# Optimization experiments

Hardware: AMD Instinct MI355X
Metric: run time of the kernel (lower is better)

## Reference

```python
import jax, jax.numpy as jnp
import numpy as np

N, H, W = 4096, 96, 96
C0 = 0.28209479177387814
C1 = 0.4886025119029199
C2 = [1.0925484305920792, -1.0925484305920792, 0.31539156525252005, -1.0925484305920792, 0.5462742152960396]
C3 = [-0.5900435899266435, 2.890611442640554, -0.4570457994644658, 0.3731763325901154, -0.4570457994644658, 1.445305721320277, -0.5900435899266435]


def setup_inputs() -> dict:
    key = jax.random.key(0)
    ks = jax.random.split(key, 6)
    return {
        'pws': jax.random.normal(ks[0], (N, 3), jnp.float32),
        'low_shs': 0.5 * jax.random.normal(ks[1], (N, 3), jnp.float32),
        'high_shs': 0.1 * jax.random.normal(ks[2], (N, 45), jnp.float32),
        'alphas_raw': jax.random.normal(ks[3], (N, 1), jnp.float32),
        'scales_raw': 0.5 * jax.random.normal(ks[4], (N, 3), jnp.float32) - 3.0,
        'rots_raw': jax.random.normal(ks[5], (N, 4), jnp.float32),
        'us': jnp.zeros((N, 2), jnp.float32),
        'Rcw': jnp.eye(3, dtype=jnp.float32),
        'tcw': jnp.array([0.0, 0.0, 4.0], jnp.float32),
        'cam_intr': jnp.array([120.0, 120.0, 48.0, 48.0], jnp.float32),  # fx fy cx cy
    }


def quat_to_rot(q):
    w, x, y, z = q[:, 0], q[:, 1], q[:, 2], q[:, 3]
    return jnp.stack([
        jnp.stack([1 - 2 * (y * y + z * z), 2 * (x * y - w * z), 2 * (x * z + w * y)], -1),
        jnp.stack([2 * (x * y + w * z), 1 - 2 * (x * x + z * z), 2 * (y * z - w * x)], -1),
        jnp.stack([2 * (x * z - w * y), 2 * (y * z + w * x), 1 - 2 * (x * x + y * y)], -1),
    ], -2)  # [N,3,3]


def sh2color(shs, dirs):
    # shs [N,16,3], dirs [N,3] normalized view directions
    x, y, z = dirs[:, 0:1], dirs[:, 1:2], dirs[:, 2:3]
    xx, yy, zz = x * x, y * y, z * z
    xy, yz, xz = x * y, y * z, x * z
    c = C0 * shs[:, 0]
    c = c - C1 * y * shs[:, 1] + C1 * z * shs[:, 2] - C1 * x * shs[:, 3]
    c = (c + C2[0] * xy * shs[:, 4] + C2[1] * yz * shs[:, 5]
         + C2[2] * (2 * zz - xx - yy) * shs[:, 6]
         + C2[3] * xz * shs[:, 7] + C2[4] * (xx - yy) * shs[:, 8])
    c = (c + C3[0] * y * (3 * xx - yy) * shs[:, 9] + C3[1] * xy * z * shs[:, 10]
         + C3[2] * y * (4 * zz - xx - yy) * shs[:, 11]
         + C3[3] * z * (2 * zz - 3 * xx - 3 * yy) * shs[:, 12]
         + C3[4] * x * (4 * zz - xx - yy) * shs[:, 13]
         + C3[5] * z * (xx - yy) * shs[:, 14]
         + C3[6] * x * (xx - 3 * yy) * shs[:, 15])
    return jnp.maximum(c + 0.5, 0.0)  # [N,3]


def _forward(pws, low_shs, high_shs, alphas_raw, scales_raw, rots_raw, Rcw, tcw, cam_intr):
    fx, fy, cx, cy = cam_intr[0], cam_intr[1], cam_intr[2], cam_intr[3]
    alphas = jax.nn.sigmoid(alphas_raw)[:, 0]                 # get_alphas
    scales = jnp.exp(scales_raw)                              # get_scales
    rots = rots_raw / jnp.linalg.norm(rots_raw, axis=1, keepdims=True)  # get_rots
    shs = jnp.concatenate([low_shs, high_shs], axis=1).reshape(-1, 16, 3)

    # --- project ---
    pcs = pws @ Rcw.T + tcw                                   # [N,3] camera coords
    depths = pcs[:, 2]
    zs = jnp.where(depths > 1e-6, depths, 1e-6)
    u = jnp.stack([fx * pcs[:, 0] / zs + cx, fy * pcs[:, 1] / zs + cy], axis=1)

    # --- cov3d = (R S)(R S)^T ---
    M = quat_to_rot(rots) * scales[:, None, :]
    cov3d = M @ jnp.swapaxes(M, 1, 2)                          # [N,3,3]

    # --- cov2d = J W cov3d W^T J^T + 0.3 I ---
    limx, limy = 1.3 * (W / (2.0 * fx)), 1.3 * (H / (2.0 * fy))
    tx = jnp.clip(pcs[:, 0] / zs, -limx, limx) * zs
    ty = jnp.clip(pcs[:, 1] / zs, -limy, limy) * zs
    zero = jnp.zeros_like(zs)
    J = jnp.stack([
        jnp.stack([fx / zs, zero, -fx * tx / (zs * zs)], -1),
        jnp.stack([zero, fy / zs, -fy * ty / (zs * zs)], -1),
    ], -2)                                                     # [N,2,3]
    T = J @ Rcw
    cov2d = T @ cov3d @ jnp.swapaxes(T, 1, 2)
    a = cov2d[:, 0, 0] + 0.3
    b = cov2d[:, 0, 1]
    c2 = cov2d[:, 1, 1] + 0.3

    # --- inverseCov2D + areas (radius of 3-sigma ellipse) ---
    det = a * c2 - b * b
    cinv = jnp.stack([c2, -b, a], axis=1) / det[:, None]       # [N,3]
    mid = 0.5 * (a + c2)
    lam = mid + jnp.sqrt(jnp.maximum(mid * mid - det, 0.1))
    radius = jnp.ceil(3.0 * jnp.sqrt(lam))
    areas = jnp.stack([radius, radius], axis=1)                # [N,2]

    # --- sh2Color ---
    twc = -(Rcw.T @ tcw)
    dirs = pws - twc
    dirs = dirs / jnp.linalg.norm(dirs, axis=1, keepdims=True)
    colors = sh2color(shs, dirs)                               # [N,3]

    # --- splat: depth-sorted alpha compositing ---
    valid = depths > 0.2
    order = jnp.argsort(depths)
    u_s, cinv_s = u[order], cinv[order]
    alpha_s, color_s, valid_s = alphas[order], colors[order], valid[order]

    px = (jnp.arange(W, dtype=jnp.float32))[None, :].repeat(H, 0).reshape(-1)
    py = (jnp.arange(H, dtype=jnp.float32))[:, None].repeat(W, 1).reshape(-1)
    dx = u_s[:, 0:1] - px[None, :]                             # [N,P]
    dy = u_s[:, 1:2] - py[None, :]
    power = -0.5 * (cinv_s[:, 0:1] * dx * dx + cinv_s[:, 2:3] * dy * dy) - cinv_s[:, 1:2] * dx * dy
    ap = jnp.minimum(alpha_s[:, None] * jnp.exp(jnp.minimum(power, 0.0)), 0.99)
    ap = jnp.where((ap >= 1.0 / 255.0) & valid_s[:, None], ap, 0.0)
    logt = jnp.cumsum(jnp.log1p(-ap), axis=0)
    tau = jnp.exp(jnp.concatenate([jnp.zeros((1, ap.shape[1])), logt[:-1]], axis=0))
    wgt = jnp.where(tau > 1e-4, ap * tau, 0.0)                 # [N,P]
    image = jnp.einsum('nc,np->cp', color_s, wgt).reshape(3, H, W)
    return image, areas


def reference(pws, low_shs, high_shs, alphas_raw, scales_raw, rots_raw, us, Rcw, tcw, cam_intr):
    return _forward(pws, low_shs, high_shs, alphas_raw, scales_raw, rots_raw, Rcw, tcw, cam_intr)
```

## Files before the change

kernel.cpp:

```cpp
#include <hip/hip_runtime.h>
#include <hip/hip_bf16.h>
#include <math.h>

#define GS_N 4096
#define IMG_H 96
#define IMG_W 96
#define NPIX (IMG_H * IMG_W)
#define TILE_PX 12
#define TILES_X 8
#define NTILES (TILES_X * TILES_X)
#define WAVES_PER_TILE 36

#define SH_C0 0.28209479177387814f
#define SH_C1 0.4886025119029199f
__device__ __constant__ float kC2[5] = {1.0925484305920792f, -1.0925484305920792f, 0.31539156525252005f, -1.0925484305920792f, 0.5462742152960396f};
__device__ __constant__ float kC3[7] = {-0.5900435899266435f, 2.890611442640554f, -0.4570457994644658f, 0.3731763325901154f, -0.4570457994644658f, 1.445305721320277f, -0.5900435899266435f};

__global__ __launch_bounds__(256) void gs_prep(
    const float* __restrict__ pws, const float* __restrict__ low_shs,
    const float* __restrict__ high_shs, const float* __restrict__ alphas_raw,
    const float* __restrict__ scales_raw, const float* __restrict__ rots_raw,
    const float* __restrict__ Rcw, const float* __restrict__ tcw,
    const float* __restrict__ cam,
    float* __restrict__ areas_out,
    float* __restrict__ depth_ws,
    int*   __restrict__ rank_ws,
    float4* __restrict__ A_uns,
    float4* __restrict__ B_uns,
    float* __restrict__ C_uns,
    float4* __restrict__ D_uns)
{
    int i = blockIdx.x * 256 + threadIdx.x;
    if (i >= GS_N) return;

    rank_ws[i] = 0;

    float fx = cam[0], fy = cam[1], cxi = cam[2], cyi = cam[3];
    float R0 = Rcw[0], R1 = Rcw[1], R2 = Rcw[2];
    float R3 = Rcw[3], R4 = Rcw[4], R5 = Rcw[5];
    float R6 = Rcw[6], R7 = Rcw[7], R8 = Rcw[8];
    float t0 = tcw[0], t1 = tcw[1], t2 = tcw[2];

    float pwx = pws[3*i+0], pwy = pws[3*i+1], pwz = pws[3*i+2];

    float pcx = R0*pwx + R1*pwy + R2*pwz + t0;
    float pcy = R3*pwx + R4*pwy + R5*pwz + t1;
    float pcz = R6*pwx + R7*pwy + R8*pwz + t2;

    float depth = pcz;
    float zs = (depth > 1e-6f) ? depth : 1e-6f;

    float ux = fx * pcx / zs + cxi;
    float uy = fy * pcy / zs + cyi;

    float alpha = 1.0f / (1.0f + expf(-alphas_raw[i]));

    float s0 = expf(scales_raw[3*i+0]);
    float s1 = expf(scales_raw[3*i+1]);
    float s2 = expf(scales_raw[3*i+2]);

    float qw = rots_raw[4*i+0], qx = rots_raw[4*i+1], qy = rots_raw[4*i+2], qz = rots_raw[4*i+3];
    float qn = sqrtf(qw*qw + qx*qx + qy*qy + qz*qz);
    qw /= qn; qx /= qn; qy /= qn; qz /= qn;

    float r00 = 1.0f - 2.0f*(qy*qy + qz*qz);
    float r01 = 2.0f*(qx*qy - qw*qz);
    float r02 = 2.0f*(qx*qz + qw*qy);
    float r10 = 2.0f*(qx*qy + qw*qz);
    float r11 = 1.0f - 2.0f*(qx*qx + qz*qz);
    float r12 = 2.0f*(qy*qz - qw*qx);
    float r20 = 2.0f*(qx*qz - qw*qy);
    float r21 = 2.0f*(qy*qz + qw*qx);
    float r22 = 1.0f - 2.0f*(qx*qx + qy*qy);

    float m00 = r00*s0, m01 = r01*s1, m02 = r02*s2;
    float m10 = r10*s0, m11 = r11*s1, m12 = r12*s2;
    float m20 = r20*s0, m21 = r21*s1, m22 = r22*s2;

    float V00 = m00*m00 + m01*m01 + m02*m02;
    float V01 = m00*m10 + m01*m11 + m02*m12;
    float V02 = m00*m20 + m01*m21 + m02*m22;
    float V11 = m10*m10 + m11*m11 + m12*m12;
    float V12 = m10*m20 + m11*m21 + m12*m22;
    float V22 = m20*m20 + m21*m21 + m22*m22;

    float limx = 1.3f * ((float)IMG_W / (2.0f * fx));
    float limy = 1.3f * ((float)IMG_H / (2.0f * fy));
    float xzr = pcx / zs, yzr = pcy / zs;
    float txv = fminf(fmaxf(xzr, -limx), limx) * zs;
    float tyv = fminf(fmaxf(yzr, -limy), limy) * zs;

    float J00 = fx / zs, J02 = -fx * txv / (zs * zs);
    float J11 = fy / zs, J12 = -fy * tyv / (zs * zs);

    float T00 = J00*R0 + J02*R6, T01 = J00*R1 + J02*R7, T02 = J00*R2 + J02*R8;
    float T10 = J11*R3 + J12*R6, T11 = J11*R4 + J12*R7, T12 = J11*R5 + J12*R8;

    float TW00 = T00*V00 + T01*V01 + T02*V02;
    float TW01 = T00*V01 + T01*V11 + T02*V12;
    float TW02 = T00*V02 + T01*V12 + T02*V22;
    float TW10 = T10*V00 + T11*V01 + T12*V02;
    float TW11 = T10*V01 + T11*V11 + T12*V12;
    float TW12 = T10*V02 + T11*V12 + T12*V22;

    float c00 = TW00*T00 + TW01*T01 + TW02*T02;
    float c01 = TW00*T10 + TW01*T11 + TW02*T12;
    float c11 = TW10*T10 + TW11*T11 + TW12*T12;

    float a  = c00 + 0.3f;
    float b  = c01;
    float cc = c11 + 0.3f;
    float det = a * cc - b * b;
    float ci0 = cc / det;
    float ci1 = -b / det;
    float ci2 = a / det;

    float mid = 0.5f * (a + cc);
    float lam = mid + sqrtf(fmaxf(mid * mid - det, 0.1f));
    float radius = ceilf(3.0f * sqrtf(lam));
    areas_out[2*i + 0] = radius;
    areas_out[2*i + 1] = radius;

    float twcx = -(R0*t0 + R3*t1 + R6*t2);
    float twcy = -(R1*t0 + R4*t1 + R7*t2);
    float twcz = -(R2*t0 + R5*t1 + R8*t2);
    float dx = pwx - twcx, dy = pwy - twcy, dz = pwz - twcz;
    float dn = sqrtf(dx*dx + dy*dy + dz*dz);
    dx /= dn; dy /= dn; dz /= dn;

    float xx = dx*dx, yy = dy*dy, zz = dz*dz;
    float xy = dx*dy, yz = dy*dz, xz = dx*dz;

    float bas0  = SH_C0;
    float bas1  = -SH_C1 * dy;
    float bas2  =  SH_C1 * dz;
    float bas3  = -SH_C1 * dx;
    float bas4  = kC2[0] * xy;
    float bas5  = kC2[1] * yz;
    float bas6  = kC2[2] * (2.0f*zz - xx - yy);
    float bas7  = kC2[3] * xz;
    float bas8  = kC2[4] * (xx - yy);
    float bas9  = kC3[0] * dy * (3.0f*xx - yy);
    float bas10 = kC3[1] * xy * dz;
    float bas11 = kC3[2] * dy * (4.0f*zz - xx - yy);
    float bas12 = kC3[3] * dz * (2.0f*zz - 3.0f*xx - 3.0f*yy);
    float bas13 = kC3[4] * dx * (4.0f*zz - xx - yy);
    float bas14 = kC3[5] * dz * (xx - yy);
    float bas15 = kC3[6] * dx * (xx - 3.0f*yy);

    float col[3];
    #pragma unroll
    for (int c = 0; c < 3; ++c) {
        const float* hs = high_shs + 45*i + c;
        float acc = bas0 * low_shs[3*i + c];
        acc += bas1  * hs[0*3];
        acc += bas2  * hs[1*3];
        acc += bas3  * hs[2*3];
        acc += bas4  * hs[3*3];
        acc += bas5  * hs[4*3];
        acc += bas6  * hs[5*3];
        acc += bas7  * hs[6*3];
        acc += bas8  * hs[7*3];
        acc += bas9  * hs[8*3];
        acc += bas10 * hs[9*3];
        acc += bas11 * hs[10*3];
        acc += bas12 * hs[11*3];
        acc += bas13 * hs[12*3];
        acc += bas14 * hs[13*3];
        acc += bas15 * hs[14*3];
        col[c] = fmaxf(acc + 0.5f, 0.0f);
    }

    bool valid = depth > 0.2f;
    float al_eff = valid ? alpha : 0.0f;

    float Tthr = __logf(255.0f * al_eff) + 1e-4f;
    float rx = (Tthr > 0.0f) ? sqrtf(2.0f * Tthr * a)  : -1.0f;
    float ry = (Tthr > 0.0f) ? sqrtf(2.0f * Tthr * cc) : -1.0f;

    depth_ws[i] = depth;
    A_uns[i] = make_float4(ux, uy, ci0, ci1);
    B_uns[i] = make_float4(ci2, al_eff, col[0], col[1]);
    C_uns[i] = col[2];
    D_uns[i] = make_float4(ux, uy, rx, ry);
}

__global__ __launch_bounds__(256) void gs_rank_partial(
    const float* __restrict__ depth, int* __restrict__ rank_ws)
{
    __shared__ float sd[256];
    int itile = blockIdx.x >> 4;
    int jtile = blockIdx.x & 15;
    int tid = threadIdx.x;
    int i = itile * 256 + tid;

    sd[tid] = depth[jtile * 256 + tid];
    __syncthreads();

    float mg = depth[i];
    int jbase = jtile * 256;
    int rank = 0;
    const float4* s4 = (const float4*)sd;
    #pragma unroll 16
    for (int jj = 0; jj < 64; ++jj) {
        float4 v = s4[jj];
        int j0 = jbase + jj * 4;
        rank += (v.x < mg || (v.x == mg && (j0+0) < i)) ? 1 : 0;
        rank += (v.y < mg || (v.y == mg && (j0+1) < i)) ? 1 : 0;
        rank += (v.z < mg || (v.z == mg && (j0+2) < i)) ? 1 : 0;
        rank += (v.w < mg || (v.w == mg && (j0+3) < i)) ? 1 : 0;
    }
    atomicAdd(&rank_ws[i], rank);
}

__global__ __launch_bounds__(256) void gs_gather(
    const int* __restrict__ rank_ws,
    const float4* __restrict__ A_uns, const float4* __restrict__ B_uns,
    const float* __restrict__ C_uns, const float4* __restrict__ D_uns,
    float4* __restrict__ A_s, float4* __restrict__ B_s, float* __restrict__ C_s,
    float4* __restrict__ D_s)
{
    int i = blockIdx.x * 256 + threadIdx.x;
    int r = rank_ws[i];
    A_s[r] = A_uns[i];
    B_s[r] = B_uns[i];
    C_s[r] = C_uns[i];
    D_s[r] = D_uns[i];
}

__global__ __launch_bounds__(256) void gs_bin(
    const float4* __restrict__ D_s,
    int* __restrict__ tile_list, int* __restrict__ tile_cnt)
{
    __shared__ int s_base;
    __shared__ int warp_off[4];
    int tile = blockIdx.x;
    int tx = tile & (TILES_X - 1), ty = tile >> 3;
    float x0 = (float)(tx * TILE_PX), x1 = (float)(tx * TILE_PX + TILE_PX - 1);
    float y0 = (float)(ty * TILE_PX), y1 = (float)(ty * TILE_PX + TILE_PX - 1);

    int tid = threadIdx.x;
    int lane = tid & 63, w = tid >> 6;
    if (tid == 0) s_base = 0;
    __syncthreads();

    int* list = tile_list + tile * GS_N;

    for (int r = 0; r < GS_N / 256; ++r) {
        int g = r * 256 + tid;
        float4 d = D_s[g];
        bool pred = (d.z >= 0.0f) &&
                    (d.x - d.z <= x1) && (d.x + d.z >= x0) &&
                    (d.y - d.w <= y1) && (d.y + d.w >= y0);
        unsigned long long m = __ballot(pred);
        int before = __popcll(m & ((1ull << lane) - 1ull));
        int wcnt = __popcll(m);
        if (lane == 0) warp_off[w] = wcnt;
        __syncthreads();
        int off = s_base;
        #pragma unroll
        for (int k = 0; k < 4; ++k) if (k < w) off += warp_off[k];
        if (pred) list[off + before] = g;
        __syncthreads();
        if (tid == 0) s_base += warp_off[0] + warp_off[1] + warp_off[2] + warp_off[3];
    }
    __syncthreads();
    if (tid == 0) tile_cnt[tile] = s_base;
}

__global__ __launch_bounds__(256) void gs_raster(
    const float4* __restrict__ A_s, const float4* __restrict__ B_s,
    const float* __restrict__ C_s,
    const int* __restrict__ tile_list, const int* __restrict__ tile_cnt,
    float* __restrict__ img)
{
    int b = blockIdx.x;
    int tile = b / WAVES_PER_TILE;
    int sub  = b - tile * WAVES_PER_TILE;
    int lane = threadIdx.x & 63;
    int wv   = threadIdx.x >> 6;

    int idxp = sub * 4 + wv;
    int lx = idxp % TILE_PX, ly = idxp / TILE_PX;
    int tx = tile & (TILES_X - 1), ty = tile >> 3;
    int pxi = tx * TILE_PX + lx, pyi = ty * TILE_PX + ly;
    float px = (float)pxi, py = (float)pyi;
    int p = pyi * IMG_W + pxi;

    int cnt = tile_cnt[tile];
    const int* list = tile_list + tile * GS_N;

    float carry = 1.0f;
    float accr = 0.0f, accg = 0.0f, accb = 0.0f;

    for (int c0 = 0; c0 < cnt; c0 += 64) {
        int k = c0 + lane;
        float ap = 0.0f, colr = 0.0f, colg = 0.0f, colb = 0.0f;
        if (k < cnt) {
            int n = list[k];
            float4 a4 = A_s[n];
            float4 b4 = B_s[n];
            colb = C_s[n];
            colr = b4.z; colg = b4.w;

            float ddx = a4.x - px;
            float ddy = a4.y - py;
            float pw = -0.5f * (a4.z * ddx * ddx + b4.x * ddy * ddy) - a4.w * ddx * ddy;
            pw = fminf(pw, 0.0f);
            ap = b4.y * __expf(pw);
            ap = fminf(ap, 0.99f);
            ap = (ap >= (1.0f / 255.0f)) ? ap : 0.0f;
        }

        float f = 1.0f - ap;
        float incl = f;
        #pragma unroll
        for (int d = 1; d < 64; d <<= 1) {
            float v = __shfl_up(incl, d, 64);
            if (lane >= d) incl *= v;
        }
        float excl = __shfl_up(incl, 1, 64);
        if (lane == 0) excl = 1.0f;

        float tau = carry * excl;
        float wgt = (tau > 1e-4f) ? ap * tau : 0.0f;
        accr += colr * wgt;
        accg += colg * wgt;
        accb += colb * wgt;

        carry *= __shfl(incl, 63, 64);
        if (carry <= 1e-4f) break;
    }

    #pragma unroll
    for (int d = 32; d >= 1; d >>= 1) {
        accr += __shfl_xor(accr, d, 64);
        accg += __shfl_xor(accg, d, 64);
        accb += __shfl_xor(accb, d, 64);
    }
    if (lane == 0) {
        img[0 * NPIX + p] = accr;
        img[1 * NPIX + p] = accg;
        img[2 * NPIX + p] = accb;
    }
}

extern "C" void kernel_launch(void* const* d_in, const int* in_sizes, int n_in,
                              void* d_out, int out_size, void* d_ws, size_t ws_size,
                              hipStream_t stream) {
    const float* pws        = (const float*)d_in[0];
    const float* low_shs    = (const float*)d_in[1];
    const float* high_shs   = (const float*)d_in[2];
    const float* alphas_raw = (const float*)d_in[3];
    const float* scales_raw = (const float*)d_in[4];
    const float* rots_raw   = (const float*)d_in[5];
    const float* Rcw        = (const float*)d_in[7];
    const float* tcw        = (const float*)d_in[8];
    const float* cam        = (const float*)d_in[9];

    float* out_img   = (float*)d_out;
    float* out_areas = (float*)d_out + 3 * NPIX;

    char* ws = (char*)d_ws;
    float*  depth_ws = (float*) (ws + 0);
    int*    rank_ws  = (int*)   (ws + 16384);
    float4* A_uns    = (float4*)(ws + 32768);
    float4* B_uns    = (float4*)(ws + 98304);
    float*  C_uns    = (float*) (ws + 163840);
    float4* D_uns    = (float4*)(ws + 180224);
    float4* A_s      = (float4*)(ws + 245760);
    float4* B_s      = (float4*)(ws + 311296);
    float*  C_s      = (float*) (ws + 376832);
    float4* D_s      = (float4*)(ws + 393216);
    int*    tile_cnt = (int*)   (ws + 458752);
    int*    tile_list= (int*)   (ws + 460800);

    gs_prep<<<GS_N / 256, 256, 0, stream>>>(
        pws, low_shs, high_shs, alphas_raw, scales_raw, rots_raw, Rcw, tcw, cam,
        out_areas, depth_ws, rank_ws, A_uns, B_uns, C_uns, D_uns);

    gs_rank_partial<<<256, 256, 0, stream>>>(depth_ws, rank_ws);

    gs_gather<<<GS_N / 256, 256, 0, stream>>>(
        rank_ws, A_uns, B_uns, C_uns, D_uns, A_s, B_s, C_s, D_s);

    gs_bin<<<NTILES, 256, 0, stream>>>(D_s, tile_list, tile_cnt);

    gs_raster<<<NTILES * WAVES_PER_TILE, 256, 0, stream>>>(
        A_s, B_s, C_s, tile_list, tile_cnt, out_img);
}
```

Before: 102.7 us.

## Replace global depth sort and gather with per-tile sort inside binning

```diff
diff --git a/kernel.cpp b/kernel.cpp
--- a/kernel.cpp
+++ b/kernel.cpp
@@ -24,7 +24,6 @@
     const float* __restrict__ cam,
     float* __restrict__ areas_out,
     float* __restrict__ depth_ws,
-    int*   __restrict__ rank_ws,
     float4* __restrict__ A_uns,
     float4* __restrict__ B_uns,
     float* __restrict__ C_uns,
@@ -32,8 +31,6 @@
 {
     int i = blockIdx.x * 256 + threadIdx.x;
     if (i >= GS_N) return;
-
-    rank_ws[i] = 0;
 
     float fx = cam[0], fy = cam[1], cxi = cam[2], cyi = cam[3];
     float R0 = Rcw[0], R1 = Rcw[1], R2 = Rcw[2];
@@ -185,55 +182,15 @@
     D_uns[i] = make_float4(ux, uy, rx, ry);
 }
 
-__global__ __launch_bounds__(256) void gs_rank_partial(
-    const float* __restrict__ depth, int* __restrict__ rank_ws)
-{
-    __shared__ float sd[256];
-    int itile = blockIdx.x >> 4;
-    int jtile = blockIdx.x & 15;
-    int tid = threadIdx.x;
-    int i = itile * 256 + tid;
-
-    sd[tid] = depth[jtile * 256 + tid];
-    __syncthreads();
-
-    float mg = depth[i];
-    int jbase = jtile * 256;
-    int rank = 0;
-    const float4* s4 = (const float4*)sd;
-    #pragma unroll 16
-    for (int jj = 0; jj < 64; ++jj) {
-        float4 v = s4[jj];
-        int j0 = jbase + jj * 4;
-        rank += (v.x < mg || (v.x == mg && (j0+0) < i)) ? 1 : 0;
-        rank += (v.y < mg || (v.y == mg && (j0+1) < i)) ? 1 : 0;
-        rank += (v.z < mg || (v.z == mg && (j0+2) < i)) ? 1 : 0;
-        rank += (v.w < mg || (v.w == mg && (j0+3) < i)) ? 1 : 0;
-    }
-    atomicAdd(&rank_ws[i], rank);
-}
-
-__global__ __launch_bounds__(256) void gs_gather(
-    const int* __restrict__ rank_ws,
-    const float4* __restrict__ A_uns, const float4* __restrict__ B_uns,
-    const float* __restrict__ C_uns, const float4* __restrict__ D_uns,
-    float4* __restrict__ A_s, float4* __restrict__ B_s, float* __restrict__ C_s,
-    float4* __restrict__ D_s)
-{
-    int i = blockIdx.x * 256 + threadIdx.x;
-    int r = rank_ws[i];
-    A_s[r] = A_uns[i];
-    B_s[r] = B_uns[i];
-    C_s[r] = C_uns[i];
-    D_s[r] = D_uns[i];
-}
-
-__global__ __launch_bounds__(256) void gs_bin(
-    const float4* __restrict__ D_s,
+__global__ __launch_bounds__(256) void gs_bin_sort(
+    const float4* __restrict__ D_uns, const float* __restrict__ depth_ws,
     int* __restrict__ tile_list, int* __restrict__ tile_cnt)
 {
+    __shared__ __align__(16) float sdep[GS_N + 4];
+    __shared__ int   sidx[GS_N];
     __shared__ int s_base;
     __shared__ int warp_off[4];
+
     int tile = blockIdx.x;
     int tx = tile & (TILES_X - 1), ty = tile >> 3;
     float x0 = (float)(tx * TILE_PX), x1 = (float)(tx * TILE_PX + TILE_PX - 1);
@@ -244,11 +201,9 @@
     if (tid == 0) s_base = 0;
     __syncthreads();
 
-    int* list = tile_list + tile * GS_N;
-
     for (int r = 0; r < GS_N / 256; ++r) {
         int g = r * 256 + tid;
-        float4 d = D_s[g];
+        float4 d = D_uns[g];
         bool pred = (d.z >= 0.0f) &&
                     (d.x - d.z <= x1) && (d.x + d.z >= x0) &&
                     (d.y - d.w <= y1) && (d.y + d.w >= y0);
@@ -260,17 +215,37 @@
         int off = s_base;
         #pragma unroll
         for (int k = 0; k < 4; ++k) if (k < w) off += warp_off[k];
-        if (pred) list[off + before] = g;
+        if (pred) { sdep[off + before] = depth_ws[g]; sidx[off + before] = g; }
         __syncthreads();
         if (tid == 0) s_base += warp_off[0] + warp_off[1] + warp_off[2] + warp_off[3];
     }
     __syncthreads();
-    if (tid == 0) tile_cnt[tile] = s_base;
+    int cnt = s_base;
+    if (tid < 4) sdep[cnt + tid] = INFINITY;
+    __syncthreads();
+
+    int* list = tile_list + tile * GS_N;
+    int cnt4 = (cnt + 3) >> 2;
+    const float4* s4 = (const float4*)sdep;
+    for (int e = tid; e < cnt; e += 256) {
+        float de = sdep[e];
+        int rank = 0;
+        for (int jj = 0; jj < cnt4; ++jj) {
+            float4 v = s4[jj];
+            int j0 = jj * 4;
+            rank += (v.x < de || (v.x == de && (j0+0) < e)) ? 1 : 0;
+            rank += (v.y < de || (v.y == de && (j0+1) < e)) ? 1 : 0;
+            rank += (v.z < de || (v.z == de && (j0+2) < e)) ? 1 : 0;
+            rank += (v.w < de || (v.w == de && (j0+3) < e)) ? 1 : 0;
+        }
+        list[rank] = sidx[e];
+    }
+    if (tid == 0) tile_cnt[tile] = cnt;
 }
 
 __global__ __launch_bounds__(256) void gs_raster(
-    const float4* __restrict__ A_s, const float4* __restrict__ B_s,
-    const float* __restrict__ C_s,
+    const float4* __restrict__ A_uns, const float4* __restrict__ B_uns,
+    const float* __restrict__ C_uns,
     const int* __restrict__ tile_list, const int* __restrict__ tile_cnt,
     float* __restrict__ img)
 {
@@ -298,9 +273,9 @@
         float ap = 0.0f, colr = 0.0f, colg = 0.0f, colb = 0.0f;
         if (k < cnt) {
             int n = list[k];
-            float4 a4 = A_s[n];
-            float4 b4 = B_s[n];
-            colb = C_s[n];
+            float4 a4 = A_uns[n];
+            float4 b4 = B_uns[n];
+            colb = C_uns[n];
             colr = b4.z; colg = b4.w;
 
             float ddx = a4.x - px;
@@ -363,29 +338,19 @@
 
     char* ws = (char*)d_ws;
     float*  depth_ws = (float*) (ws + 0);
-    int*    rank_ws  = (int*)   (ws + 16384);
-    float4* A_uns    = (float4*)(ws + 32768);
-    float4* B_uns    = (float4*)(ws + 98304);
-    float*  C_uns    = (float*) (ws + 163840);
-    float4* D_uns    = (float4*)(ws + 180224);
-    float4* A_s      = (float4*)(ws + 245760);
-    float4* B_s      = (float4*)(ws + 311296);
-    float*  C_s      = (float*) (ws + 376832);
-    float4* D_s      = (float4*)(ws + 393216);
-    int*    tile_cnt = (int*)   (ws + 458752);
-    int*    tile_list= (int*)   (ws + 460800);
+    float4* A_uns    = (float4*)(ws + 16384);
+    float4* B_uns    = (float4*)(ws + 81920);
+    float*  C_uns    = (float*) (ws + 147456);
+    float4* D_uns    = (float4*)(ws + 163840);
+    int*    tile_cnt = (int*)   (ws + 229376);
+    int*    tile_list= (int*)   (ws + 231424);
 
     gs_prep<<<GS_N / 256, 256, 0, stream>>>(
         pws, low_shs, high_shs, alphas_raw, scales_raw, rots_raw, Rcw, tcw, cam,
-        out_areas, depth_ws, rank_ws, A_uns, B_uns, C_uns, D_uns);
-
-    gs_rank_partial<<<256, 256, 0, stream>>>(depth_ws, rank_ws);
-
-    gs_gather<<<GS_N / 256, 256, 0, stream>>>(
-        rank_ws, A_uns, B_uns, C_uns, D_uns, A_s, B_s, C_s, D_s);
-
-    gs_bin<<<NTILES, 256, 0, stream>>>(D_s, tile_list, tile_cnt);
+        out_areas, depth_ws, A_uns, B_uns, C_uns, D_uns);
+
+    gs_bin_sort<<<NTILES, 256, 0, stream>>>(D_uns, depth_ws, tile_list, tile_cnt);
 
     gs_raster<<<NTILES * WAVES_PER_TILE, 256, 0, stream>>>(
-        A_s, B_s, C_s, tile_list, tile_cnt, out_img);
+        A_uns, B_uns, C_uns, tile_list, tile_cnt, out_img);
 }
```

After: 116.2 us. 1.13x slower.
